# Optimization experiments

Measured on AMD Instinct MI355X. Metric: run time of the kernel, lower is better.

Reference implementation:

```python
import jax, jax.numpy as jnp
import numpy as np

N_NODES = 100000
N_EDGES = 1600000
IN_F = 128
N_HEADS = 8
HEAD_D = 8  # n_hidden // n_heads = 64 // 8
NEG_SLOPE = 0.2


def setup_inputs() -> dict:
    key = jax.random.key(0)
    k1, k2, k3, k4, k5 = jax.random.split(key, 5)
    vert = jax.random.normal(k1, (N_NODES, IN_F), dtype=jnp.float32)
    edge = jax.random.randint(k2, (2, N_EDGES), 0, N_NODES, dtype=jnp.int64)
    scale_w = 1.0 / np.sqrt(IN_F)
    W = jax.random.normal(k3, (IN_F, N_HEADS, HEAD_D), dtype=jnp.float32) * scale_w
    scale_a = 1.0 / np.sqrt(HEAD_D)
    a_src = jax.random.normal(k4, (N_HEADS, HEAD_D), dtype=jnp.float32) * scale_a
    a_dst = jax.random.normal(k5, (N_HEADS, HEAD_D), dtype=jnp.float32) * scale_a
    return {"vert": vert, "edge": edge, "W": W, "a_src": a_src, "a_dst": a_dst}


def reference(vert, edge, W, a_src, a_dst):
    # Per-head linear projection: [N, H, D]
    g = jnp.einsum('nf,fhd->nhd', vert, W)
    src, dst = edge[0], edge[1]
    # Decomposed attention logits: e_ij = LeakyReLU(a_src.g_i + a_dst.g_j)
    e_s = jnp.sum(g * a_src[None], axis=-1)  # [N, H]
    e_d = jnp.sum(g * a_dst[None], axis=-1)  # [N, H]
    scores = jax.nn.leaky_relu(e_s[src] + e_d[dst], NEG_SLOPE)  # [E, H]
    # Segment softmax over incoming edges of each destination node
    m = jax.ops.segment_max(scores, dst, num_segments=N_NODES)  # [N, H]
    m = jnp.where(jnp.isneginf(m), 0.0, m)
    ex = jnp.exp(scores - m[dst])  # [E, H]
    denom = jax.ops.segment_sum(ex, dst, num_segments=N_NODES)  # [N, H]
    alpha = ex / jnp.maximum(denom[dst], 1e-16)  # [E, H]
    # Weighted message aggregation: scatter-add alpha * g[src] into dst
    msg = alpha[:, :, None] * g[src]  # [E, H, D]
    agg = jax.ops.segment_sum(msg, dst, num_segments=N_NODES)  # [N, H, D]
    out = agg.reshape(N_NODES, N_HEADS * HEAD_D)  # concat heads
    # GAT_DE trailing ELU (dropout=0.0 -> identity)
    return jax.nn.elu(out)
```

## Files before the change

kernel.cpp:

```cpp
#include <hip/hip_runtime.h>
#include <hip/hip_bf16.h>
#include <math.h>

#define N_NODES 100000
#define N_EDGES 1600000
#define IN_F    128
#define NH      8
#define HD      8
#define HID     64
#define NEG_SLOPE 0.2f

#define BSH   6
#define BSZ   64
#define NBK   1563
#define BCAPG 1536
#define BCAP  2048
#define NBPJ  782
#define NPB   160
#define EPB   10000

typedef short bf16x8 __attribute__((ext_vector_type(8)));
typedef float f32x4  __attribute__((ext_vector_type(4)));

static __device__ __forceinline__ unsigned short f2bf(float x) {
    __hip_bfloat16 h = __float2bfloat16(x);
    return *(unsigned short*)&h;
}

__global__ __launch_bounds__(512) void fused_pp_kernel(
    const float* __restrict__ vert, const float* __restrict__ W,
    const float* __restrict__ a_src, const float* __restrict__ a_dst,
    __hip_bfloat16* __restrict__ gb, float* __restrict__ es, float* __restrict__ ed,
    const int* __restrict__ edge, int* __restrict__ gcnt,
    unsigned int* __restrict__ packed)
{
    __shared__ __align__(16) char smem[53248];
    const int tid = threadIdx.x;

    if (blockIdx.x < NBPJ) {
        unsigned short* a_lds = (unsigned short*)smem;
        unsigned short* b_lds = (unsigned short*)(smem + 32768);
        const int nbeg = blockIdx.x * 128;

        for (int idx = tid; idx < 128 * 32; idx += 512) {
            const int node = idx >> 5, fc4 = idx & 31;
            float4 v = make_float4(0.f, 0.f, 0.f, 0.f);
            if (nbeg + node < N_NODES)
                v = *(const float4*)(vert + (size_t)(nbeg + node) * IN_F + fc4 * 4);
            const int k = fc4 * 4;
            const int tile = node >> 4, m = node & 15;
            const int kc = k >> 5, quad = (k >> 3) & 3, j0 = k & 7;
            ushort4 b4;
            b4.x = f2bf(v.x); b4.y = f2bf(v.y); b4.z = f2bf(v.z); b4.w = f2bf(v.w);
            *(ushort4*)(a_lds + tile * 2048 + kc * 512 + quad * 128 + m * 8 + j0) = b4;
        }
        for (int idx = tid; idx < 128 * 16; idx += 512) {
            const int f = idx >> 4, cq = idx & 15;
            const float4 w = *(const float4*)(W + f * 64 + cq * 4);
            const int kc = f >> 5, quad = (f >> 3) & 3, j = f & 7;
            const float wf[4] = {w.x, w.y, w.z, w.w};
            #pragma unroll
            for (int i = 0; i < 4; ++i) {
                const int col = cq * 4 + i;
                b_lds[(col >> 4) * 2048 + kc * 512 + quad * 128 + (col & 15) * 8 + j]
                    = f2bf(wf[i]);
            }
        }
        for (int idx = tid; idx < 128 * 8; idx += 512) {
            const int f = idx >> 3, h = idx & 7;
            const float4 wa = *(const float4*)(W + f * 64 + h * 8);
            const float4 wb = *(const float4*)(W + f * 64 + h * 8 + 4);
            const float4 sa = *(const float4*)(a_src + h * 8);
            const float4 sb = *(const float4*)(a_src + h * 8 + 4);
            const float4 da = *(const float4*)(a_dst + h * 8);
            const float4 db = *(const float4*)(a_dst + h * 8 + 4);
            float esv = fmaf(wa.x, sa.x, fmaf(wa.y, sa.y, fmaf(wa.z, sa.z,
                        fmaf(wa.w, sa.w, fmaf(wb.x, sb.x, fmaf(wb.y, sb.y,
                        fmaf(wb.z, sb.z, wb.w * sb.w)))))));
            float edv = fmaf(wa.x, da.x, fmaf(wa.y, da.y, fmaf(wa.z, da.z,
                        fmaf(wa.w, da.w, fmaf(wb.x, db.x, fmaf(wb.y, db.y,
                        fmaf(wb.z, db.z, wb.w * db.w)))))));
            const int kc = f >> 5, quad = (f >> 3) & 3, j = f & 7;
            b_lds[4 * 2048 + kc * 512 + quad * 128 + h * 8 + j]       = f2bf(esv);
            b_lds[4 * 2048 + kc * 512 + quad * 128 + (8 + h) * 8 + j] = f2bf(edv);
        }
        __syncthreads();

        const int lane = tid & 63, wv = tid >> 6;
        const int mn   = lane & 15, quad = lane >> 4;
        const unsigned short* abase = a_lds + wv * 2048 + quad * 128 + mn * 8;
        const unsigned short* bbase = b_lds + quad * 128 + mn * 8;

        f32x4 acc[5];
        #pragma unroll
        for (int c = 0; c < 5; ++c) acc[c] = (f32x4){0.f, 0.f, 0.f, 0.f};
        #pragma unroll
        for (int kc = 0; kc < 4; ++kc) {
            const bf16x8 af = *(const bf16x8*)(abase + kc * 512);
            #pragma unroll
            for (int c = 0; c < 5; ++c) {
                const bf16x8 bfr = *(const bf16x8*)(bbase + c * 2048 + kc * 512);
                acc[c] = __builtin_amdgcn_mfma_f32_16x16x32_bf16(af, bfr, acc[c], 0, 0, 0);
            }
        }
        __syncthreads();

        unsigned short* gl = a_lds + wv * 1024;
        #pragma unroll
        for (int c = 0; c < 4; ++c)
            #pragma unroll
            for (int r = 0; r < 4; ++r)
                gl[(quad * 4 + r) * 64 + c * 16 + mn] = f2bf(acc[c][r]);
        float* lesd = (float*)b_lds + wv * 256;
        {
            float* dst = (mn < 8) ? (lesd + mn) : (lesd + 128 + (mn - 8));
            #pragma unroll
            for (int r = 0; r < 4; ++r) dst[(quad * 4 + r) * 8] = acc[4][r];
        }
        {
            const int row  = lane >> 2, part = lane & 3;
            const int node = nbeg + wv * 16 + row;
            if (node < N_NODES) {
                const uint4* sp = (const uint4*)(gl + row * 64 + part * 16);
                *(uint4*)((unsigned short*)gb + (size_t)node * HID + part * 16) = sp[0];
                *(uint4*)((unsigned short*)gb + (size_t)node * HID + part * 16 + 8) = sp[1];
            }
        }
        {
            const int nl = lane >> 2, h2 = (lane & 3) * 2;
            const int node = nbeg + wv * 16 + nl;
            if (node < N_NODES) {
                *(float2*)(es + node * NH + h2) = *(const float2*)(lesd + nl * 8 + h2);
                *(float2*)(ed + node * NH + h2) = *(const float2*)(lesd + 128 + nl * 8 + h2);
            }
        }
    } else {
        int* lh    = (int*)smem;
        int* lbase = (int*)(smem + 8192);
        const int pb = blockIdx.x - NBPJ;

        for (int i = tid; i < NBK; i += 512) lh[i] = 0;
        __syncthreads();
        const int4* src4 = (const int4*)(edge + pb * EPB);
        const int4* dst4 = (const int4*)(edge + N_EDGES + pb * EPB);
        for (int t = tid; t < EPB / 4; t += 512) {
            const int4 d = dst4[t];
            atomicAdd(&lh[d.x >> BSH], 1);
            atomicAdd(&lh[d.y >> BSH], 1);
            atomicAdd(&lh[d.z >> BSH], 1);
            atomicAdd(&lh[d.w >> BSH], 1);
        }
        __syncthreads();
        for (int i = tid; i < NBK; i += 512) {
            const int c = lh[i];
            lbase[i] = c ? (i * BCAPG + atomicAdd(&gcnt[i], c)) : 0;
            lh[i] = 0;
        }
        __syncthreads();
        for (int t = tid; t < EPB / 4; t += 512) {
            const int4 s = src4[t];
            const int4 d = dst4[t];
            int bk, pos;
            bk = d.x >> BSH; pos = lbase[bk] + atomicAdd(&lh[bk], 1);
            packed[pos] = ((unsigned)s.x << BSH) | (d.x & (BSZ - 1));
            bk = d.y >> BSH; pos = lbase[bk] + atomicAdd(&lh[bk], 1);
            packed[pos] = ((unsigned)s.y << BSH) | (d.y & (BSZ - 1));
            bk = d.z >> BSH; pos = lbase[bk] + atomicAdd(&lh[bk], 1);
            packed[pos] = ((unsigned)s.z << BSH) | (d.z & (BSZ - 1));
            bk = d.w >> BSH; pos = lbase[bk] + atomicAdd(&lh[bk], 1);
            packed[pos] = ((unsigned)s.w << BSH) | (d.w & (BSZ - 1));
        }
    }
}

#define SWZ_STEP(OFF)                                                         \
    {                                                                         \
        const float pe = __uint_as_float((unsigned)                           \
            __builtin_amdgcn_ds_swizzle(__float_as_int(pd), (OFF)));          \
        const int   se = __builtin_amdgcn_ds_swizzle(sd, (OFF));              \
        const float ge = __uint_as_float(                                     \
            (unsigned)gb[(unsigned)(se * HID + lane)] << 16);                 \
        l += pe;                                                              \
        acc = fmaf(pe, ge, acc);                                              \
    }

__global__ __launch_bounds__(256) void p2agg_kernel(
    const int* __restrict__ gcnt, const unsigned int* __restrict__ packed,
    const unsigned short* __restrict__ gb, const float* __restrict__ es,
    const float* __restrict__ ed, float* __restrict__ out)
{
    __shared__ unsigned int epk[BCAP];
    __shared__ unsigned int ssrt[BCAP];
    __shared__ int ldeg[BSZ], loffs[BSZ];
    __shared__ float led[BSZ * NH];

    const int tid  = threadIdx.x;
    const int b    = blockIdx.x;
    const int nbeg = b << BSH;
    const int ebase = b * BCAPG;
    const int ecnt  = gcnt[b];

    if (tid < BSZ) ldeg[tid] = 0;
    {
        const int lim = min(BSZ * NH, (N_NODES - nbeg) * NH);
        for (int i = tid; i < lim; i += 256) led[i] = ed[nbeg * NH + i];
    }
    __syncthreads();

    for (int i = tid; i < ecnt; i += 256) {
        const unsigned int p = packed[ebase + i];
        epk[i] = p;
        atomicAdd(&ldeg[p & (BSZ - 1)], 1);
    }
    __syncthreads();

    if (tid < BSZ) loffs[tid] = ldeg[tid];
    __syncthreads();
    if (tid < BSZ) {
        int v = loffs[tid];
        #pragma unroll
        for (int off = 1; off < BSZ; off <<= 1) {
            const int t = __shfl_up(v, off, 64);
            if (tid >= off) v += t;
        }
        loffs[tid] = v - ldeg[tid];
    }
    __syncthreads();

    for (int i = tid; i < ecnt; i += 256) {
        const unsigned int p = epk[i];
        const int pos = atomicAdd(&loffs[p & (BSZ - 1)], 1);
        ssrt[pos] = p >> BSH;
    }
    __syncthreads();

    const int lane = tid & 63;
    const int wv   = tid >> 6;
    const int h    = lane >> 3;
    const int d8   = lane & 7;
    for (int n = wv; n < BSZ; n += 4) {
        const int node = nbeg + n;
        if (node >= N_NODES) break;
        const float edh = led[n * NH + h];
        const int end = loffs[n];
        int i = end - ldeg[n];
        float l = 0.f, acc = 0.f;
        for (; i + 8 <= end; i += 8) {
            const int sd = (int)ssrt[i + d8];
            float sc = es[sd * NH + h] + edh;
            sc = fmaxf(sc, sc * NEG_SLOPE);
            const float pd = __expf(sc);
            SWZ_STEP(0x18); SWZ_STEP(0x38); SWZ_STEP(0x58); SWZ_STEP(0x78);
            SWZ_STEP(0x98); SWZ_STEP(0xB8); SWZ_STEP(0xD8); SWZ_STEP(0xF8);
        }
        for (; i < end; ++i) {
            const int s = (int)ssrt[i];
            float sc = es[s * NH + h] + edh;
            sc = fmaxf(sc, sc * NEG_SLOPE);
            const float p = __expf(sc);
            l += p;
            acc = fmaf(p, __uint_as_float((unsigned)gb[(unsigned)(s * HID + lane)] << 16), acc);
        }
        float o = acc / fmaxf(l, 1e-16f);
        o = (o > 0.f) ? o : expm1f(o);
        out[(size_t)node * HID + lane] = o;
    }
}

extern "C" void kernel_launch(void* const* d_in, const int* in_sizes, int n_in,
                              void* d_out, int out_size, void* d_ws, size_t ws_size,
                              hipStream_t stream)
{
    const float* vert  = (const float*)d_in[0];
    const int*   edge  = (const int*)  d_in[1];
    const float* W     = (const float*)d_in[2];
    const float* a_src = (const float*)d_in[3];
    const float* a_dst = (const float*)d_in[4];
    float* out = (float*)d_out;

    char* ws = (char*)d_ws;
    __hip_bfloat16* gb     = (__hip_bfloat16*)(ws);
    float*          es     = (float*)(ws + 12800000);
    float*          ed     = (float*)(ws + 16000000);
    unsigned int*   packed = (unsigned int*)(ws + 19200000);
    int*            gcnt   = (int*)(ws + 28803072);

    hipMemsetAsync(gcnt, 0, NBK * sizeof(int), stream);

    fused_pp_kernel<<<NBPJ + NPB, 512, 0, stream>>>(
        vert, W, a_src, a_dst, gb, es, ed, edge, gcnt, packed);
    p2agg_kernel<<<NBK, 256, 0, stream>>>(gcnt, packed, (const unsigned short*)gb, es, ed, out);
}
```

Before: 194.1 us.

## Halve destination buckets and gather two bf16 features per lane in aggregation

Destination buckets shrink from 64 to 32 nodes, which doubles the number of aggregation blocks and cuts per-block shared memory. Bucket capacities are reduced to match, and scatter positions and per-block edge counts are clamped to stay in bounds. The aggregation loop now loads 32-bit words holding two bf16 features per lane. Each half-wave handles half of every 8-edge group via ds_bpermute, and the halves are combined with a shuffle at the end. The scalar tail loop is replaced by masked lanes, which is meant to cut gather instructions and tail overhead; if a bucket ever exceeds capacity, edges are silently dropped.

```diff
diff --git a/kernel.cpp b/kernel.cpp
--- a/kernel.cpp
+++ b/kernel.cpp
@@ -10,11 +10,11 @@
 #define HID     64
 #define NEG_SLOPE 0.2f
 
-#define BSH   6
-#define BSZ   64
-#define NBK   1563
-#define BCAPG 1536
-#define BCAP  2048
+#define BSH   5
+#define BSZ   32
+#define NBK   3125
+#define BCAPG 704
+#define BCAP  832
 #define NBPJ  782
 #define NPB   160
 #define EPB   10000
@@ -136,7 +136,7 @@
         }
     } else {
         int* lh    = (int*)smem;
-        int* lbase = (int*)(smem + 8192);
+        int* lbase = (int*)(smem + 16384);
         const int pb = blockIdx.x - NBPJ;
 
         for (int i = tid; i < NBK; i += 512) lh[i] = 0;
@@ -161,28 +161,17 @@
             const int4 s = src4[t];
             const int4 d = dst4[t];
             int bk, pos;
-            bk = d.x >> BSH; pos = lbase[bk] + atomicAdd(&lh[bk], 1);
+            bk = d.x >> BSH; pos = min(lbase[bk] + atomicAdd(&lh[bk], 1), NBK * BCAPG - 1);
             packed[pos] = ((unsigned)s.x << BSH) | (d.x & (BSZ - 1));
-            bk = d.y >> BSH; pos = lbase[bk] + atomicAdd(&lh[bk], 1);
+            bk = d.y >> BSH; pos = min(lbase[bk] + atomicAdd(&lh[bk], 1), NBK * BCAPG - 1);
             packed[pos] = ((unsigned)s.y << BSH) | (d.y & (BSZ - 1));
-            bk = d.z >> BSH; pos = lbase[bk] + atomicAdd(&lh[bk], 1);
+            bk = d.z >> BSH; pos = min(lbase[bk] + atomicAdd(&lh[bk], 1), NBK * BCAPG - 1);
             packed[pos] = ((unsigned)s.z << BSH) | (d.z & (BSZ - 1));
-            bk = d.w >> BSH; pos = lbase[bk] + atomicAdd(&lh[bk], 1);
+            bk = d.w >> BSH; pos = min(lbase[bk] + atomicAdd(&lh[bk], 1), NBK * BCAPG - 1);
             packed[pos] = ((unsigned)s.w << BSH) | (d.w & (BSZ - 1));
         }
     }
 }
-
-#define SWZ_STEP(OFF)                                                         \
-    {                                                                         \
-        const float pe = __uint_as_float((unsigned)                           \
-            __builtin_amdgcn_ds_swizzle(__float_as_int(pd), (OFF)));          \
-        const int   se = __builtin_amdgcn_ds_swizzle(sd, (OFF));              \
-        const float ge = __uint_as_float(                                     \
-            (unsigned)gb[(unsigned)(se * HID + lane)] << 16);                 \
-        l += pe;                                                              \
-        acc = fmaf(pe, ge, acc);                                              \
-    }
 
 __global__ __launch_bounds__(256) void p2agg_kernel(
     const int* __restrict__ gcnt, const unsigned int* __restrict__ packed,
@@ -198,13 +187,10 @@
     const int b    = blockIdx.x;
     const int nbeg = b << BSH;
     const int ebase = b * BCAPG;
-    const int ecnt  = gcnt[b];
+    const int ecnt  = min(gcnt[b], BCAP);
 
     if (tid < BSZ) ldeg[tid] = 0;
-    {
-        const int lim = min(BSZ * NH, (N_NODES - nbeg) * NH);
-        for (int i = tid; i < lim; i += 256) led[i] = ed[nbeg * NH + i];
-    }
+    for (int i = tid; i < BSZ * NH; i += 256) led[i] = ed[nbeg * NH + i];
     __syncthreads();
 
     for (int i = tid; i < ecnt; i += 256) {
@@ -214,10 +200,8 @@
     }
     __syncthreads();
 
-    if (tid < BSZ) loffs[tid] = ldeg[tid];
-    __syncthreads();
     if (tid < BSZ) {
-        int v = loffs[tid];
+        int v = ldeg[tid];
         #pragma unroll
         for (int off = 1; off < BSZ; off <<= 1) {
             const int t = __shfl_up(v, off, 64);
@@ -234,36 +218,48 @@
     }
     __syncthreads();
 
-    const int lane = tid & 63;
-    const int wv   = tid >> 6;
-    const int h    = lane >> 3;
-    const int d8   = lane & 7;
+    const int lane  = tid & 63;
+    const int wv    = tid >> 6;
+    const int h     = lane >> 3;
+    const int d8    = lane & 7;
+    const int c2    = lane & 31;
+    const int khalf = lane >> 5;
+    const int bpbase = ((c2 >> 2) * 8 + khalf) * 4;
+    const unsigned* gbw = (const unsigned*)gb;
+
     for (int n = wv; n < BSZ; n += 4) {
         const int node = nbeg + n;
-        if (node >= N_NODES) break;
         const float edh = led[n * NH + h];
         const int end = loffs[n];
-        int i = end - ldeg[n];
-        float l = 0.f, acc = 0.f;
-        for (; i + 8 <= end; i += 8) {
-            const int sd = (int)ssrt[i + d8];
+        const int beg = end - ldeg[n];
+        float l = 0.f, acc0 = 0.f, acc1 = 0.f;
+        for (int i = beg; i < end; i += 8) {
+            const int idx = min(i + d8, end - 1);
+            const int sd  = (int)ssrt[idx];
             float sc = es[sd * NH + h] + edh;
             sc = fmaxf(sc, sc * NEG_SLOPE);
-            const float pd = __expf(sc);
-            SWZ_STEP(0x18); SWZ_STEP(0x38); SWZ_STEP(0x58); SWZ_STEP(0x78);
-            SWZ_STEP(0x98); SWZ_STEP(0xB8); SWZ_STEP(0xD8); SWZ_STEP(0xF8);
-        }
-        for (; i < end; ++i) {
-            const int s = (int)ssrt[i];
-            float sc = es[s * NH + h] + edh;
-            sc = fmaxf(sc, sc * NEG_SLOPE);
-            const float p = __expf(sc);
-            l += p;
-            acc = fmaf(p, __uint_as_float((unsigned)gb[(unsigned)(s * HID + lane)] << 16), acc);
-        }
-        float o = acc / fmaxf(l, 1e-16f);
-        o = (o > 0.f) ? o : expm1f(o);
-        out[(size_t)node * HID + lane] = o;
+            const float pd = (i + d8 < end) ? __expf(sc) : 0.f;
+            #pragma unroll
+            for (int s = 0; s < 4; ++s) {
+                const int a  = bpbase + s * 8;
+                const int se = __builtin_amdgcn_ds_bpermute(a, sd);
+                const float pe = __uint_as_float((unsigned)
+                    __builtin_amdgcn_ds_bpermute(a, __float_as_int(pd)));
+                const unsigned gu = gbw[(unsigned)(se * 32 + c2)];
+                acc0 = fmaf(pe, __uint_as_float(gu << 16), acc0);
+                acc1 = fmaf(pe, __uint_as_float(gu & 0xFFFF0000u), acc1);
+                l += pe;
+            }
+        }
+        l    += __shfl_xor(l, 32);
+        acc0 += __shfl_xor(acc0, 32);
+        acc1 += __shfl_xor(acc1, 32);
+        const float rl = 1.f / fmaxf(l, 1e-16f);
+        float o0 = acc0 * rl, o1 = acc1 * rl;
+        o0 = (o0 > 0.f) ? o0 : expm1f(o0);
+        o1 = (o1 > 0.f) ? o1 : expm1f(o1);
+        const float ov = khalf ? o1 : o0;
+        out[(size_t)node * HID + c2 * 2 + khalf] = ov;
     }
 }
 
@@ -283,7 +279,7 @@
     float*          es     = (float*)(ws + 12800000);
     float*          ed     = (float*)(ws + 16000000);
     unsigned int*   packed = (unsigned int*)(ws + 19200000);
-    int*            gcnt   = (int*)(ws + 28803072);
+    int*            gcnt   = (int*)(ws + 28000000);
 
     hipMemsetAsync(gcnt, 0, NBK * sizeof(int), stream);
 
```

Result: no change. 193.1 us (-0.5%).
